# Kernel tuning notes

Measured on AMD Instinct MI355X. Metric: run time of the kernel, lower is better.

Reference implementation:

```python
import jax, jax.numpy as jnp
import numpy as np
import math

B, T_IN, T_COND, D, H, W = 2, 2048, 1024, 1024, 16, 512
HD = D // H
NEG = -1e9


def setup_inputs() -> dict:
    key = jax.random.key(0)
    ks = jax.random.split(key, 6)
    scale = 0.02
    x = jax.random.normal(ks[0], (B, T_IN, D), dtype=jnp.float32)
    condition = jax.random.normal(ks[1], (B, T_COND, D), dtype=jnp.float32)
    end_inds = jax.random.randint(ks[2], (B,), W, min(T_IN, T_COND), dtype=jnp.int32)
    in_proj_w = jax.random.normal(ks[3], (3 * D, D), dtype=jnp.float32) * scale
    in_proj_b = jnp.zeros((3 * D,), dtype=jnp.float32)
    out_w = jax.random.normal(ks[4], (D, D), dtype=jnp.float32) * scale
    out_b = jnp.zeros((D,), dtype=jnp.float32)
    return {"x": x, "condition": condition, "end_inds": end_inds,
            "in_proj_w": in_proj_w, "in_proj_b": in_proj_b,
            "out_w": out_w, "out_b": out_b}


def _window_mask(end_inds, t_in, t_cond):
    # allowed keys: index in [end - W, end) within each of the two segments
    e = end_inds[:, None].astype(jnp.int32)
    idx_in = jnp.arange(t_in, dtype=jnp.int32)[None, :]
    idx_c = jnp.arange(t_cond, dtype=jnp.int32)[None, :]
    m_in = (idx_in >= e - W) & (idx_in < e)
    m_c = (idx_c >= e - W) & (idx_c < e)
    return jnp.concatenate([m_in, m_c], axis=1)  # (B, S)


def reference(x, condition, end_inds, in_proj_w, in_proj_b, out_w, out_b):
    inp = jnp.concatenate([x, condition], axis=1)          # (B, S, D)
    S = inp.shape[1]
    qkv = inp @ in_proj_w.T + in_proj_b                     # (B, S, 3D)
    q, k, v = jnp.split(qkv, 3, axis=-1)
    # (B, H, S, HD)
    q = q.reshape(B, S, H, HD).transpose(0, 2, 1, 3)
    k = k.reshape(B, S, H, HD).transpose(0, 2, 1, 3)
    v = v.reshape(B, S, H, HD).transpose(0, 2, 1, 3)
    scores = jnp.einsum('bhqd,bhkd->bhqk', q, k) / math.sqrt(HD)
    mask = _window_mask(end_inds, x.shape[1], condition.shape[1])  # (B, S)
    scores = jnp.where(mask[:, None, None, :], scores, NEG)
    attn = jax.nn.softmax(scores, axis=-1)
    out = jnp.einsum('bhqk,bhkd->bhqd', attn, v)            # (B, H, S, HD)
    out = out.transpose(0, 2, 1, 3).reshape(B, S, D)
    return out @ out_w.T + out_b
```

## Files before the change

kernel.cpp:

```cpp
#include <hip/hip_runtime.h>
#include <stdint.h>

#define TIN   2048
#define TCOND 1024
#define SEQ   3072
#define NB    2
#define NH    16
#define DM    1024
#define HDIM  64
#define WIN   512
#define MROWS (NB*SEQ)
#define NQKV  (3*DM)

typedef float  floatx4 __attribute__((ext_vector_type(4)));
typedef short  bf16x8  __attribute__((ext_vector_type(8)));

__device__ __forceinline__ unsigned short f2bf(float f) {
    unsigned int u = __float_as_uint(f);
    u += 0x7fffu + ((u >> 16) & 1u);
    return (unsigned short)(u >> 16);
}

__device__ __forceinline__ unsigned int pack2bf(float a, float b) {
    return (unsigned int)f2bf(a) | ((unsigned int)f2bf(b) << 16);
}

__device__ __forceinline__ void gl2lds16(const void* g, void* l) {
    __builtin_amdgcn_global_load_lds(
        (const __attribute__((address_space(1))) unsigned int*)g,
        (__attribute__((address_space(3))) unsigned int*)l, 16, 0, 0);
}

__global__ __launch_bounds__(256) void prep(const float* __restrict__ x,
                                            const float* __restrict__ cond,
                                            const float* __restrict__ w_in,
                                            const float* __restrict__ w_out,
                                            unsigned short* __restrict__ inp,
                                            unsigned short* __restrict__ wi_bf,
                                            unsigned short* __restrict__ wo_bf) {
    if (blockIdx.x < 6144) {
        int v = blockIdx.x * 256 + threadIdx.x;
        int m  = v >> 8;
        int d4 = v & 255;
        int bb = (m >= SEQ) ? 1 : 0;
        int s  = m - bb * SEQ;
        const float* src = (s < TIN)
            ? x    + ((size_t)(bb * TIN   + s)        ) * DM + d4 * 4
            : cond + ((size_t)(bb * TCOND + (s - TIN))) * DM + d4 * 4;
        float4 f = *(const float4*)src;
        ushort4 u;
        u.x = f2bf(f.x); u.y = f2bf(f.y); u.z = f2bf(f.z); u.w = f2bf(f.w);
        *(ushort4*)(inp + (size_t)v * 4) = u;
    } else {
        int v = (blockIdx.x - 6144) * 256 + threadIdx.x;
        const float* src; unsigned short* dst; int idx;
        if (v < 786432) { src = w_in;  dst = wi_bf; idx = v; }
        else            { src = w_out; dst = wo_bf; idx = v - 786432; }
        float4 f = *(const float4*)(src + (size_t)idx * 4);
        ushort4 u;
        u.x = f2bf(f.x); u.y = f2bf(f.y); u.z = f2bf(f.z); u.w = f2bf(f.w);
        *(ushort4*)(dst + (size_t)idx * 4) = u;
    }
}

template<int EPI>
__global__ __launch_bounds__(256) void gemm_bt(
        const unsigned short* __restrict__ A, const unsigned short* __restrict__ Bt,
        int M, int N, int K,
        const float* __restrict__ bias,
        unsigned short* __restrict__ q_ws, unsigned short* __restrict__ k_ws,
        unsigned short* __restrict__ vt_ws, float* __restrict__ outp) {
    __shared__ unsigned short smem[2 * 8192];
    const int tid  = threadIdx.x;
    const int wave = tid >> 6, lane = tid & 63;
    const int quad = lane >> 4, c16 = lane & 15;
    const int wr = wave >> 1, wc = wave & 1;
    const int m0 = blockIdx.y * 128, n0 = blockIdx.x * 128;

    const unsigned short* gA[2];
    const unsigned short* gB[2];
    int ldst[2];
#pragma unroll
    for (int i = 0; i < 2; i++) {
        int flat = i * 256 + tid;
        int pr = flat >> 2, cp = flat & 3;
        int gc = cp ^ ((pr >> 1) & 3);
        gA[i] = A  + (size_t)(m0 + pr) * K + (gc << 3);
        gB[i] = Bt + (size_t)(n0 + pr) * K + (gc << 3);
        ldst[i] = (i * 256 + wave * 64) * 8;
    }

    floatx4 acc[4][4];
#pragma unroll
    for (int i = 0; i < 4; i++)
#pragma unroll
        for (int j = 0; j < 4; j++) acc[i][j] = (floatx4){0.f, 0.f, 0.f, 0.f};

    const int NIT = K >> 5;
#pragma unroll
    for (int i = 0; i < 2; i++) {
        gl2lds16(gA[i], &smem[ldst[i]]);
        gl2lds16(gB[i], &smem[4096 + ldst[i]]);
    }

    for (int it = 0; it < NIT; ++it) {
        __syncthreads();
        if (it + 1 < NIT) {
            int buf = (it + 1) & 1;
            int k0 = (it + 1) << 5;
#pragma unroll
            for (int i = 0; i < 2; i++) {
                gl2lds16(gA[i] + k0, &smem[buf * 8192 + ldst[i]]);
                gl2lds16(gB[i] + k0, &smem[buf * 8192 + 4096 + ldst[i]]);
            }
        }
        const unsigned short* As = &smem[(it & 1) * 8192];
        const unsigned short* Bs = As + 4096;
        bf16x8 af[4], bfr[4];
#pragma unroll
        for (int t = 0; t < 4; t++) {
            int ra = wr * 64 + t * 16 + c16;
            int rb = wc * 64 + t * 16 + c16;
            af[t]  = *(const bf16x8*)&As[ra * 32 + ((quad ^ ((ra >> 1) & 3)) << 3)];
            bfr[t] = *(const bf16x8*)&Bs[rb * 32 + ((quad ^ ((rb >> 1) & 3)) << 3)];
        }
#pragma unroll
        for (int mt = 0; mt < 4; mt++)
#pragma unroll
            for (int nt = 0; nt < 4; nt++)
                acc[mt][nt] = __builtin_amdgcn_mfma_f32_16x16x32_bf16(
                    af[mt], bfr[nt], acc[mt][nt], 0, 0, 0);
    }

    if (EPI == 0) {
        const int which = n0 >> 10;
        const int h0 = (n0 >> 6) & 15;
        if (which == 2) {
#pragma unroll
            for (int mt = 0; mt < 4; mt++) {
                int m = m0 + wr * 64 + mt * 16 + quad * 4;
                int bb = (m >= SEQ) ? 1 : 0;
                int s = m - bb * SEQ;
#pragma unroll
                for (int nt = 0; nt < 4; nt++) {
                    int gn = n0 + wc * 64 + nt * 16 + c16;
                    float bi = bias[gn];
                    int h = (gn >> 6) & 15, hd = gn & 63;
                    uint2 w;
                    w.x = pack2bf(acc[mt][nt][0] + bi, acc[mt][nt][1] + bi);
                    w.y = pack2bf(acc[mt][nt][2] + bi, acc[mt][nt][3] + bi);
                    *(uint2*)&vt_ws[((size_t)(bb * NH + h) * HDIM + hd) * SEQ + s] = w;
                }
            }
        } else {
            unsigned short* dstb = (which == 0) ? q_ws : k_ws;
            const float qs = (which == 0) ? 0.125f : 1.0f;
#pragma unroll
            for (int mt = 0; mt < 4; mt++) {
                __syncthreads();
#pragma unroll
                for (int nt = 0; nt < 4; nt++) {
                    int col = wc * 64 + nt * 16 + c16;
                    float bi = bias[n0 + col];
#pragma unroll
                    for (int r = 0; r < 4; r++)
                        smem[(wr * 16 + quad * 4 + r) * 136 + col] =
                            f2bf((acc[mt][nt][r] + bi) * qs);
                }
                __syncthreads();
#pragma unroll
                for (int p = 0; p < 2; p++) {
                    int flat = p * 256 + tid;
                    int row = flat >> 4, seg = flat & 15;
                    bf16x8 v = *(const bf16x8*)&smem[row * 136 + seg * 8];
                    int m = m0 + (row >> 4) * 64 + mt * 16 + (row & 15);
                    int bb = (m >= SEQ) ? 1 : 0;
                    int s = m - bb * SEQ;
                    int h = h0 + (seg >> 3);
                    *(bf16x8*)&dstb[((size_t)(bb * NH + h) * SEQ + s) * HDIM + (seg & 7) * 8] = v;
                }
            }
        }
    } else {
        float* smf = (float*)smem;
#pragma unroll
        for (int mt = 0; mt < 4; mt++) {
            __syncthreads();
#pragma unroll
            for (int nt = 0; nt < 4; nt++) {
                int col = wc * 64 + nt * 16 + c16;
                float bi = bias[n0 + col];
#pragma unroll
                for (int r = 0; r < 4; r++)
                    smf[(wr * 16 + quad * 4 + r) * 132 + col] = acc[mt][nt][r] + bi;
            }
            __syncthreads();
#pragma unroll
            for (int p = 0; p < 4; p++) {
                int flat = p * 256 + tid;
                int row = flat >> 5, seg = flat & 31;
                float4 v = *(const float4*)&smf[row * 132 + seg * 4];
                int m = m0 + (row >> 4) * 64 + mt * 16 + (row & 15);
                *(float4*)&outp[(size_t)m * DM + n0 + seg * 4] = v;
            }
        }
    }
}

__global__ __launch_bounds__(256, 2) void attn_kernel(
        const unsigned short* __restrict__ Q, const unsigned short* __restrict__ K,
        const unsigned short* __restrict__ Vt, const int* __restrict__ end_inds,
        unsigned short* __restrict__ O) {
    __shared__ unsigned short smem[2 * 16384];

    const int tid  = threadIdx.x;
    const int wave = tid >> 6, lane = tid & 63;
    const int quad = lane >> 4, c16 = lane & 15;
    const int qt = blockIdx.x, h = blockIdx.y, b = blockIdx.z;
    const int bh = b * NH + h;
    const int e  = end_inds[b];
    const int qbase = qt * 192 + wave * 48;

    const unsigned short* Qp = Q + ((size_t)bh * SEQ + qbase) * HDIM;
    bf16x8 bq[3][2];
#pragma unroll
    for (int qi = 0; qi < 3; qi++)
#pragma unroll
        for (int kk = 0; kk < 2; kk++)
            bq[qi][kk] = *(const bf16x8*)&Qp[(qi * 16 + c16) * HDIM + kk * 32 + quad * 8];

    float l_run[3] = {0.f, 0.f, 0.f};
    floatx4 accO[3][4];
#pragma unroll
    for (int qi = 0; qi < 3; qi++)
#pragma unroll
        for (int t = 0; t < 4; t++) accO[qi][t] = (floatx4){0.f, 0.f, 0.f, 0.f};

    int k_pr[4], k_src[4], v_src[4], dst_off[4];
#pragma unroll
    for (int i = 0; i < 4; i++) {
        int flat = i * 256 + tid;
        int pr = flat >> 3, cp = flat & 7;
        int m5 = pr & 31;
        int kl = (pr & ~31) + (((m5 & 15) >> 2) << 3) + (m5 & 3) + ((m5 >> 4) << 2);
        k_pr[i]  = pr;
        k_src[i] = kl * HDIM + ((cp ^ (pr & 7)) << 3);
        int vrow = flat >> 4, vcp = flat & 15;
        v_src[i] = vrow * SEQ + ((vcp ^ (vrow & 15)) << 3);
        dst_off[i] = (i * 256 + wave * 64) * 8;
    }

    const unsigned short* Kbase = K  + (size_t)bh * SEQ * HDIM;
    const unsigned short* Vbase = Vt + (size_t)bh * HDIM * SEQ;

    {
        int s0 = e - WIN;
#pragma unroll
        for (int i = 0; i < 4; i++) {
            gl2lds16(Kbase + (size_t)s0 * HDIM + k_src[i], &smem[dst_off[i]]);
            gl2lds16(Vbase + s0 + v_src[i], &smem[8192 + dst_off[i]]);
        }
    }

    for (int ch = 0; ch < 8; ch++) {
        __syncthreads();
        if (ch + 1 < 8) {
            int buf = (ch + 1) & 1;
            int cn = ch + 1;
            int s0 = (cn < 4) ? (e - WIN + cn * 128) : (TIN + e - WIN + (cn - 4) * 128);
#pragma unroll
            for (int i = 0; i < 4; i++) {
                gl2lds16(Kbase + (size_t)s0 * HDIM + k_src[i],
                         &smem[buf * 16384 + dst_off[i]]);
                gl2lds16(Vbase + s0 + v_src[i],
                         &smem[buf * 16384 + 8192 + dst_off[i]]);
            }
        }
        const unsigned short* Ks = &smem[(ch & 1) * 16384];
        const unsigned short* Vs = Ks + 8192;

#pragma unroll
        for (int u = 0; u < 4; u++) {
            unsigned int pb[3][4];
#pragma unroll
            for (int sub = 0; sub < 2; sub++) {
                int prow = u * 32 + sub * 16 + c16;
                int sw = c16 & 7;
                bf16x8 ka0 = *(const bf16x8*)&Ks[prow * 64 + (( quad      ^ sw) << 3)];
                bf16x8 ka1 = *(const bf16x8*)&Ks[prow * 64 + (((quad + 4) ^ sw) << 3)];
#pragma unroll
                for (int qi = 0; qi < 3; qi++) {
                    floatx4 z = (floatx4){0.f, 0.f, 0.f, 0.f};
                    z = __builtin_amdgcn_mfma_f32_16x16x32_bf16(ka0, bq[qi][0], z, 0, 0, 0);
                    z = __builtin_amdgcn_mfma_f32_16x16x32_bf16(ka1, bq[qi][1], z, 0, 0, 0);
                    float p0 = __expf(z[0]), p1 = __expf(z[1]);
                    float p2 = __expf(z[2]), p3 = __expf(z[3]);
                    l_run[qi] += (p0 + p1) + (p2 + p3);
                    pb[qi][sub * 2 + 0] = pack2bf(p0, p1);
                    pb[qi][sub * 2 + 1] = pack2bf(p2, p3);
                }
            }
#pragma unroll
            for (int t = 0; t < 4; t++) {
                bf16x8 va = *(const bf16x8*)&Vs[(t * 16 + c16) * 128 +
                                                (((u * 4 + quad) ^ c16) << 3)];
#pragma unroll
                for (int qi = 0; qi < 3; qi++)
                    accO[qi][t] = __builtin_amdgcn_mfma_f32_16x16x32_bf16(
                        va, *(const bf16x8*)&pb[qi][0], accO[qi][t], 0, 0, 0);
            }
        }
    }

    float inv[3];
#pragma unroll
    for (int qi = 0; qi < 3; qi++) {
        float l = l_run[qi];
        l += __shfl_xor(l, 16, 64);
        l += __shfl_xor(l, 32, 64);
        inv[qi] = 1.f / l;
    }

    __syncthreads();
    unsigned short* Os = smem + wave * (48 * 72);
#pragma unroll
    for (int qi = 0; qi < 3; qi++)
#pragma unroll
        for (int t = 0; t < 4; t++) {
            uint2 w;
            w.x = pack2bf(accO[qi][t][0] * inv[qi], accO[qi][t][1] * inv[qi]);
            w.y = pack2bf(accO[qi][t][2] * inv[qi], accO[qi][t][3] * inv[qi]);
            *(uint2*)&Os[(qi * 16 + c16) * 72 + t * 16 + quad * 4] = w;
        }
    __syncthreads();
#pragma unroll
    for (int pass = 0; pass < 6; pass++) {
        int rq = pass * 8 + (lane >> 3);
        int part = lane & 7;
        bf16x8 v = *(const bf16x8*)&Os[rq * 72 + part * 8];
        int s = qbase + rq;
        *(bf16x8*)&O[((size_t)b * SEQ + s) * DM + h * HDIM + part * 8] = v;
    }
}

extern "C" void kernel_launch(void* const* d_in, const int* in_sizes, int n_in,
                              void* d_out, int out_size, void* d_ws, size_t ws_size,
                              hipStream_t stream) {
    const float* x      = (const float*)d_in[0];
    const float* cond   = (const float*)d_in[1];
    const int*   e_inds = (const int*)d_in[2];
    const float* w_in   = (const float*)d_in[3];
    const float* b_in   = (const float*)d_in[4];
    const float* w_out  = (const float*)d_in[5];
    const float* b_out  = (const float*)d_in[6];
    float* out = (float*)d_out;

    char* ws = (char*)d_ws;
    unsigned short* inp_bf = (unsigned short*)(ws);
    unsigned short* wi_bf  = (unsigned short*)(ws + 12582912);
    unsigned short* wo_bf  = (unsigned short*)(ws + 18874368);
    unsigned short* q_ws   = (unsigned short*)(ws + 20971520);
    unsigned short* k_ws   = (unsigned short*)(ws + 33554432);
    unsigned short* vt_ws  = (unsigned short*)(ws + 46137344);
    unsigned short* o_bf   = inp_bf;

    prep<<<10240, 256, 0, stream>>>(x, cond, w_in, w_out, inp_bf, wi_bf, wo_bf);
    gemm_bt<0><<<dim3(NQKV / 128, MROWS / 128), 256, 0, stream>>>(
        inp_bf, wi_bf, MROWS, NQKV, DM, b_in, q_ws, k_ws, vt_ws, nullptr);
    attn_kernel<<<dim3(SEQ / 192, NH, NB), 256, 0, stream>>>(
        q_ws, k_ws, vt_ws, e_inds, o_bf);
    gemm_bt<1><<<dim3(DM / 128, MROWS / 128), 256, 0, stream>>>(
        o_bf, wo_bf, MROWS, DM, DM, b_out, nullptr, nullptr, nullptr, out);
}
```

Baseline: 221.9 us.

## Split GEMM into QKV kernel with 256x128 tiles and shared B tile

Replaces the templated GEMM with two specialised kernels. The QKV projection now uses 512-thread blocks covering 256x128 output tiles, so each B (weight) tile loaded into LDS is reused by twice as many rows, which cuts global weight traffic and halves the number of blocks. K is hard-coded to 1024 and both kernels carry occupancy hints in their launch bounds. The output projection stays at 128x128, and an unused k_pr array is removed from the attention kernel. The larger tile reduces the block count, which may lower wave-level parallelism and adds LDS pressure.

```diff
diff --git a/kernel.cpp b/kernel.cpp
--- a/kernel.cpp
+++ b/kernel.cpp
@@ -63,14 +63,130 @@
     }
 }
 
-template<int EPI>
-__global__ __launch_bounds__(256) void gemm_bt(
+__global__ __launch_bounds__(512, 4) void gemm_qkv(
         const unsigned short* __restrict__ A, const unsigned short* __restrict__ Bt,
-        int M, int N, int K,
         const float* __restrict__ bias,
         unsigned short* __restrict__ q_ws, unsigned short* __restrict__ k_ws,
-        unsigned short* __restrict__ vt_ws, float* __restrict__ outp) {
+        unsigned short* __restrict__ vt_ws) {
+    __shared__ unsigned short smem[2 * 12288];
+    const int K = 1024;
+    const int tid  = threadIdx.x;
+    const int wave = tid >> 6, lane = tid & 63;
+    const int quad = lane >> 4, c16 = lane & 15;
+    const int wr = wave >> 1, wc = wave & 1;
+    const int m0 = blockIdx.y * 256, n0 = blockIdx.x * 128;
+
+    const unsigned short* gA[2];
+    int ldstA[2];
+#pragma unroll
+    for (int i = 0; i < 2; i++) {
+        int flat = i * 512 + tid;
+        int pr = flat >> 2, cp = flat & 3;
+        int gc = cp ^ ((pr >> 1) & 3);
+        gA[i] = A + (size_t)(m0 + pr) * K + (gc << 3);
+        ldstA[i] = (i * 512 + wave * 64) * 8;
+    }
+    const unsigned short* gB;
+    int ldstB;
+    {
+        int pr = tid >> 2, cp = tid & 3;
+        int gc = cp ^ ((pr >> 1) & 3);
+        gB = Bt + (size_t)(n0 + pr) * K + (gc << 3);
+        ldstB = 8192 + wave * 64 * 8;
+    }
+
+    floatx4 acc[4][4];
+#pragma unroll
+    for (int i = 0; i < 4; i++)
+#pragma unroll
+        for (int j = 0; j < 4; j++) acc[i][j] = (floatx4){0.f, 0.f, 0.f, 0.f};
+
+    gl2lds16(gA[0], &smem[ldstA[0]]);
+    gl2lds16(gA[1], &smem[ldstA[1]]);
+    gl2lds16(gB,    &smem[ldstB]);
+
+    for (int it = 0; it < 32; ++it) {
+        __syncthreads();
+        if (it + 1 < 32) {
+            int bo = ((it + 1) & 1) * 12288;
+            int k0 = (it + 1) << 5;
+            gl2lds16(gA[0] + k0, &smem[bo + ldstA[0]]);
+            gl2lds16(gA[1] + k0, &smem[bo + ldstA[1]]);
+            gl2lds16(gB    + k0, &smem[bo + ldstB]);
+        }
+        const unsigned short* As = &smem[(it & 1) * 12288];
+        const unsigned short* Bs = As + 8192;
+        bf16x8 af[4], bfr[4];
+#pragma unroll
+        for (int t = 0; t < 4; t++) {
+            int ra = wr * 64 + t * 16 + c16;
+            int rb = wc * 64 + t * 16 + c16;
+            af[t]  = *(const bf16x8*)&As[ra * 32 + ((quad ^ ((ra >> 1) & 3)) << 3)];
+            bfr[t] = *(const bf16x8*)&Bs[rb * 32 + ((quad ^ ((rb >> 1) & 3)) << 3)];
+        }
+#pragma unroll
+        for (int mt = 0; mt < 4; mt++)
+#pragma unroll
+            for (int nt = 0; nt < 4; nt++)
+                acc[mt][nt] = __builtin_amdgcn_mfma_f32_16x16x32_bf16(
+                    af[mt], bfr[nt], acc[mt][nt], 0, 0, 0);
+    }
+
+    const int which = n0 >> 10;
+    const int h0 = (n0 >> 6) & 15;
+    if (which == 2) {
+#pragma unroll
+        for (int mt = 0; mt < 4; mt++) {
+            int m = m0 + wr * 64 + mt * 16 + quad * 4;
+            int bb = (m >= SEQ) ? 1 : 0;
+            int s = m - bb * SEQ;
+#pragma unroll
+            for (int nt = 0; nt < 4; nt++) {
+                int gn = n0 + wc * 64 + nt * 16 + c16;
+                float bi = bias[gn];
+                int h = (gn >> 6) & 15, hd = gn & 63;
+                uint2 w;
+                w.x = pack2bf(acc[mt][nt][0] + bi, acc[mt][nt][1] + bi);
+                w.y = pack2bf(acc[mt][nt][2] + bi, acc[mt][nt][3] + bi);
+                *(uint2*)&vt_ws[((size_t)(bb * NH + h) * HDIM + hd) * SEQ + s] = w;
+            }
+        }
+    } else {
+        unsigned short* dstb = (which == 0) ? q_ws : k_ws;
+        const float qs = (which == 0) ? 0.125f : 1.0f;
+#pragma unroll
+        for (int mt = 0; mt < 4; mt++) {
+            __syncthreads();
+#pragma unroll
+            for (int nt = 0; nt < 4; nt++) {
+                int col = wc * 64 + nt * 16 + c16;
+                float bi = bias[n0 + col];
+#pragma unroll
+                for (int r = 0; r < 4; r++)
+                    smem[(wr * 16 + quad * 4 + r) * 136 + col] =
+                        f2bf((acc[mt][nt][r] + bi) * qs);
+            }
+            __syncthreads();
+#pragma unroll
+            for (int p = 0; p < 2; p++) {
+                int flat = p * 512 + tid;
+                int row = flat >> 4, seg = flat & 15;
+                bf16x8 v = *(const bf16x8*)&smem[row * 136 + seg * 8];
+                int m = m0 + (row >> 4) * 64 + mt * 16 + (row & 15);
+                int bb = (m >= SEQ) ? 1 : 0;
+                int s = m - bb * SEQ;
+                int h = h0 + (seg >> 3);
+                *(bf16x8*)&dstb[((size_t)(bb * NH + h) * SEQ + s) * HDIM + (seg & 7) * 8] = v;
+            }
+        }
+    }
+}
+
+__global__ __launch_bounds__(256, 4) void gemm_out(
+        const unsigned short* __restrict__ A, const unsigned short* __restrict__ Bt,
+        const float* __restrict__ bias, float* __restrict__ outp) {
     __shared__ unsigned short smem[2 * 8192];
+    const int K = 1024;
     const int tid  = threadIdx.x;
     const int wave = tid >> 6, lane = tid & 63;
     const int quad = lane >> 4, c16 = lane & 15;
@@ -96,22 +212,21 @@
 #pragma unroll
         for (int j = 0; j < 4; j++) acc[i][j] = (floatx4){0.f, 0.f, 0.f, 0.f};
 
-    const int NIT = K >> 5;
 #pragma unroll
     for (int i = 0; i < 2; i++) {
         gl2lds16(gA[i], &smem[ldst[i]]);
         gl2lds16(gB[i], &smem[4096 + ldst[i]]);
     }
 
-    for (int it = 0; it < NIT; ++it) {
+    for (int it = 0; it < 32; ++it) {
         __syncthreads();
-        if (it + 1 < NIT) {
-            int buf = (it + 1) & 1;
+        if (it + 1 < 32) {
+            int bo = ((it + 1) & 1) * 8192;
             int k0 = (it + 1) << 5;
 #pragma unroll
             for (int i = 0; i < 2; i++) {
-                gl2lds16(gA[i] + k0, &smem[buf * 8192 + ldst[i]]);
-                gl2lds16(gB[i] + k0, &smem[buf * 8192 + 4096 + ldst[i]]);
+                gl2lds16(gA[i] + k0, &smem[bo + ldst[i]]);
+                gl2lds16(gB[i] + k0, &smem[bo + 4096 + ldst[i]]);
             }
         }
         const unsigned short* As = &smem[(it & 1) * 8192];
@@ -132,77 +247,26 @@
                     af[mt], bfr[nt], acc[mt][nt], 0, 0, 0);
     }
 
-    if (EPI == 0) {
-        const int which = n0 >> 10;
-        const int h0 = (n0 >> 6) & 15;
-        if (which == 2) {
-#pragma unroll
-            for (int mt = 0; mt < 4; mt++) {
-                int m = m0 + wr * 64 + mt * 16 + quad * 4;
-                int bb = (m >= SEQ) ? 1 : 0;
-                int s = m - bb * SEQ;
-#pragma unroll
-                for (int nt = 0; nt < 4; nt++) {
-                    int gn = n0 + wc * 64 + nt * 16 + c16;
-                    float bi = bias[gn];
-                    int h = (gn >> 6) & 15, hd = gn & 63;
-                    uint2 w;
-                    w.x = pack2bf(acc[mt][nt][0] + bi, acc[mt][nt][1] + bi);
-                    w.y = pack2bf(acc[mt][nt][2] + bi, acc[mt][nt][3] + bi);
-                    *(uint2*)&vt_ws[((size_t)(bb * NH + h) * HDIM + hd) * SEQ + s] = w;
-                }
-            }
-        } else {
-            unsigned short* dstb = (which == 0) ? q_ws : k_ws;
-            const float qs = (which == 0) ? 0.125f : 1.0f;
-#pragma unroll
-            for (int mt = 0; mt < 4; mt++) {
-                __syncthreads();
-#pragma unroll
-                for (int nt = 0; nt < 4; nt++) {
-                    int col = wc * 64 + nt * 16 + c16;
-                    float bi = bias[n0 + col];
-#pragma unroll
-                    for (int r = 0; r < 4; r++)
-                        smem[(wr * 16 + quad * 4 + r) * 136 + col] =
-                            f2bf((acc[mt][nt][r] + bi) * qs);
-                }
-                __syncthreads();
-#pragma unroll
-                for (int p = 0; p < 2; p++) {
-                    int flat = p * 256 + tid;
-                    int row = flat >> 4, seg = flat & 15;
-                    bf16x8 v = *(const bf16x8*)&smem[row * 136 + seg * 8];
-                    int m = m0 + (row >> 4) * 64 + mt * 16 + (row & 15);
-                    int bb = (m >= SEQ) ? 1 : 0;
-                    int s = m - bb * SEQ;
-                    int h = h0 + (seg >> 3);
-                    *(bf16x8*)&dstb[((size_t)(bb * NH + h) * SEQ + s) * HDIM + (seg & 7) * 8] = v;
-                }
-            }
-        }
-    } else {
-        float* smf = (float*)smem;
-#pragma unroll
-        for (int mt = 0; mt < 4; mt++) {
-            __syncthreads();
-#pragma unroll
-            for (int nt = 0; nt < 4; nt++) {
-                int col = wc * 64 + nt * 16 + c16;
-                float bi = bias[n0 + col];
-#pragma unroll
-                for (int r = 0; r < 4; r++)
-                    smf[(wr * 16 + quad * 4 + r) * 132 + col] = acc[mt][nt][r] + bi;
-            }
-            __syncthreads();
-#pragma unroll
-            for (int p = 0; p < 4; p++) {
-                int flat = p * 256 + tid;
-                int row = flat >> 5, seg = flat & 31;
-                float4 v = *(const float4*)&smf[row * 132 + seg * 4];
-                int m = m0 + (row >> 4) * 64 + mt * 16 + (row & 15);
-                *(float4*)&outp[(size_t)m * DM + n0 + seg * 4] = v;
-            }
+    float* smf = (float*)smem;
+#pragma unroll
+    for (int mt = 0; mt < 4; mt++) {
+        __syncthreads();
+#pragma unroll
+        for (int nt = 0; nt < 4; nt++) {
+            int col = wc * 64 + nt * 16 + c16;
+            float bi = bias[n0 + col];
+#pragma unroll
+            for (int r = 0; r < 4; r++)
+                smf[(wr * 16 + quad * 4 + r) * 132 + col] = acc[mt][nt][r] + bi;
+        }
+        __syncthreads();
+#pragma unroll
+        for (int p = 0; p < 4; p++) {
+            int flat = p * 256 + tid;
+            int row = flat >> 5, seg = flat & 31;
+            float4 v = *(const float4*)&smf[row * 132 + seg * 4];
+            int m = m0 + (row >> 4) * 64 + mt * 16 + (row & 15);
+            *(float4*)&outp[(size_t)m * DM + n0 + seg * 4] = v;
         }
     }
 }
@@ -236,14 +300,13 @@
 #pragma unroll
         for (int t = 0; t < 4; t++) accO[qi][t] = (floatx4){0.f, 0.f, 0.f, 0.f};
 
-    int k_pr[4], k_src[4], v_src[4], dst_off[4];
+    int k_src[4], v_src[4], dst_off[4];
 #pragma unroll
     for (int i = 0; i < 4; i++) {
         int flat = i * 256 + tid;
         int pr = flat >> 3, cp = flat & 7;
         int m5 = pr & 31;
         int kl = (pr & ~31) + (((m5 & 15) >> 2) << 3) + (m5 & 3) + ((m5 >> 4) << 2);
-        k_pr[i]  = pr;
         k_src[i] = kl * HDIM + ((cp ^ (pr & 7)) << 3);
         int vrow = flat >> 4, vcp = flat & 15;
         v_src[i] = vrow * SEQ + ((vcp ^ (vrow & 15)) << 3);
@@ -365,10 +428,10 @@
     unsigned short* o_bf   = inp_bf;
 
     prep<<<10240, 256, 0, stream>>>(x, cond, w_in, w_out, inp_bf, wi_bf, wo_bf);
-    gemm_bt<0><<<dim3(NQKV / 128, MROWS / 128), 256, 0, stream>>>(
-        inp_bf, wi_bf, MROWS, NQKV, DM, b_in, q_ws, k_ws, vt_ws, nullptr);
+    gemm_qkv<<<dim3(NQKV / 128, MROWS / 256), 512, 0, stream>>>(
+        inp_bf, wi_bf, b_in, q_ws, k_ws, vt_ws);
     attn_kernel<<<dim3(SEQ / 192, NH, NB), 256, 0, stream>>>(
         q_ws, k_ws, vt_ws, e_inds, o_bf);
-    gemm_bt<1><<<dim3(DM / 128, MROWS / 128), 256, 0, stream>>>(
-        o_bf, wo_bf, MROWS, DM, DM, b_out, nullptr, nullptr, nullptr, out);
-}
+    gemm_out<<<dim3(DM / 128, MROWS / 128), 256, 0, stream>>>(
+        o_bf, wo_bf, b_out, out);
+}
```

Result: faster. 209.8 us (-5.4%).
